# Kernel tuning notes

Measured on AMD Instinct MI355X. Metric: run time of the kernel, lower is better.

## Reference

```python
import jax, jax.numpy as jnp
import numpy as np

EPS = 1e-6
DIM_HEAD = 32
INP = 128
OUP = 128
IH = IW = 32


def _conv3x3(x, w):
    # NCHW conv, 3x3, stride 1, pad 1, no bias
    return jax.lax.conv_general_dilated(
        x, w, window_strides=(1, 1), padding=((1, 1), (1, 1)),
        dimension_numbers=("NCHW", "OIHW", "NCHW"))


def _groupnorm1(x, gamma, beta):
    # GroupNorm with 1 group: normalize over (C,H,W) per sample
    m = jnp.mean(x, axis=(1, 2, 3), keepdims=True)
    v = jnp.var(x, axis=(1, 2, 3), keepdims=True)
    xn = (x - m) * jax.lax.rsqrt(v + EPS)
    return xn * gamma[None, :, None, None] + beta[None, :, None, None]


def _proj(x, w, gamma, beta):
    return jax.nn.gelu(_groupnorm1(_conv3x3(x, w), gamma, beta), approximate=False)


def _relative_index(ih, iw):
    coords = np.stack(np.meshgrid(np.arange(ih), np.arange(iw), indexing="ij"))
    coords = coords.reshape(2, -1)  # (2, N)
    rel = coords[:, :, None] - coords[:, None, :]  # (2, N, N)
    rel[0] += ih - 1
    rel[1] += iw - 1
    rel[0] *= 2 * iw - 1
    return rel.sum(0).reshape(-1).astype(np.int32)  # (N*N,)


def setup_inputs() -> dict:
    key = jax.random.key(0)
    ks = jax.random.split(key, 12)
    B = 16
    x = jax.random.normal(ks[0], (B, INP, IH, IW), jnp.float32)
    w_scale = 0.05
    wq = jax.random.normal(ks[1], (INP, INP, 3, 3), jnp.float32) * w_scale
    wk = jax.random.normal(ks[2], (INP, INP, 3, 3), jnp.float32) * w_scale
    wv = jax.random.normal(ks[3], (INP, INP, 3, 3), jnp.float32) * w_scale
    gq = jnp.ones((INP,), jnp.float32); bq = jnp.zeros((INP,), jnp.float32)
    gk = jnp.ones((INP,), jnp.float32); bk = jnp.zeros((INP,), jnp.float32)
    gv = jnp.ones((INP,), jnp.float32); bv = jnp.zeros((INP,), jnp.float32)
    heads = INP // DIM_HEAD
    table = jax.random.normal(ks[4], ((2 * IH - 1) * (2 * IW - 1), heads), jnp.float32) * 0.02
    rel_index = jnp.asarray(_relative_index(IH, IW))
    out_w = jax.random.normal(ks[5], (OUP, INP, 1, 1), jnp.float32) * w_scale
    out_b = jnp.zeros((OUP,), jnp.float32)
    return {"x": x, "wq": wq, "gq": gq, "bq": bq, "wk": wk, "gk": gk, "bk": bk,
            "wv": wv, "gv": gv, "bv": bv, "table": table, "rel_index": rel_index,
            "out_w": out_w, "out_b": out_b}


def reference(x, wq, gq, bq, wk, gk, bk, wv, gv, bv, table, rel_index, out_w, out_b):
    B, C, ih, iw = x.shape
    H = C // DIM_HEAD
    N = ih * iw

    def to_heads(t):
        # b c ih iw -> b (ihiw) c -> b h n d (heads-major channel split)
        return t.reshape(B, C, N).transpose(0, 2, 1).reshape(B, N, H, DIM_HEAD).transpose(0, 2, 1, 3)

    q = to_heads(_proj(x, wq, gq, bq))
    k = to_heads(_proj(x, wk, gk, bk))
    v = to_heads(_proj(x, wv, gv, bv))

    # NOTE: original applies self.scale only when y is not None; y=None here -> no scale
    dots = jnp.einsum("bhnd,bhmd->bhnm", q, k)  # (B,H,N,N)

    bias = table[rel_index]                 # (N*N, H)
    bias = bias.reshape(N, N, H).transpose(2, 0, 1)[None]  # (1,H,N,N)
    attn = jax.nn.softmax(dots + bias, axis=-1)

    out = jnp.einsum("bhnm,bhmd->bhnd", attn, v)
    out = out.transpose(0, 2, 1, 3).reshape(B, N, C).transpose(0, 2, 1).reshape(B, C, ih, iw)
    # to_out: 1x1 conv + bias (Dropout2d is identity in eval)
    out = jax.lax.conv_general_dilated(
        out, out_w, window_strides=(1, 1), padding=((0, 0), (0, 0)),
        dimension_numbers=("NCHW", "OIHW", "NCHW")) + out_b[None, :, None, None]
    return out
```

## Files before the change

### kernel.cpp

```cpp
#include <hip/hip_runtime.h>

typedef unsigned short u16;
typedef unsigned int   u32;

#define NB   16
#define NC   128
#define NPIX 1024
#define NH   4
#define DH   32

typedef __attribute__((ext_vector_type(8))) short short8;
typedef __attribute__((ext_vector_type(4))) float f32x4;
typedef __attribute__((ext_vector_type(8))) _Float16 half8;

#define XROWS 1152

__device__ __forceinline__ float bf2f(u16 u) {
    return __uint_as_float(((u32)u) << 16);
}
__device__ __forceinline__ u16 f2bf(float f) {
    u32 u = __float_as_uint(f);
    u32 r = (u + 0x7fffu + ((u >> 16) & 1u)) >> 16;
    return (u16)r;
}
__device__ __forceinline__ u16 f2h(float f) {
    _Float16 h = (_Float16)f;
    u16 r; __builtin_memcpy(&r, &h, 2); return r;
}
__device__ __forceinline__ float h2f(u16 u) {
    _Float16 h; __builtin_memcpy(&h, &u, 2); return (float)h;
}
__device__ __forceinline__ int pk_h2(float a, float b) {
    auto h = __builtin_amdgcn_cvt_pkrtz(a, b);
    int r; __builtin_memcpy(&r, &h, 4); return r;
}
__device__ __forceinline__ float loadf(const void* p, int i, int isf) {
    return isf ? ((const float*)p)[i] : bf2f(((const u16*)p)[i]);
}
__device__ __forceinline__ float4 load4(const void* p, int i4, int isf) {
    if (isf) return ((const float4*)p)[i4];
    ushort4 u = ((const ushort4*)p)[i4];
    return make_float4(bf2f(u.x), bf2f(u.y), bf2f(u.z), bf2f(u.w));
}
__device__ __forceinline__ int detect_isf(const void* x) {
    const u16* p = (const u16*)x;
    u16 v = p[threadIdx.x & 63];
    int e = (v >> 7) & 0xFF;
    unsigned long long m = __ballot(e >= 134);
    return m != 0ull ? 1 : 0;
}

__global__ __launch_bounds__(256) void prep_all(
        const void* __restrict__ x,
        const void* __restrict__ w0, const void* __restrict__ w1,
        const void* __restrict__ w2, const void* __restrict__ ow,
        const int* __restrict__ rel, const void* __restrict__ table,
        u16* __restrict__ Wt, u16* __restrict__ Wf, u16* __restrict__ xTp,
        u16* __restrict__ biasT, float* __restrict__ stats) {
    __shared__ __align__(16) u32 smem_u[4160];
    int isf = detect_isf(x);
    int bid = blockIdx.x;
    int t = threadIdx.x;

    if (bid < 1792) {
        if (bid == 0 && t < 96) stats[t] = 0.f;
        int i = bid * 256 + t;
        if (i < 442368) {
            int j   = i / 147456;
            int rr  = i % 147456;
            int tap = rr >> 14;
            int co  = (rr >> 7) & 127;
            int ci  = rr & 127;
            const void* w = (j == 0) ? w0 : ((j == 1) ? w1 : w2);
            float v = loadf(w, (co * 128 + ci) * 9 + tap, isf);
            int coh = (co >> 6) & 1, wm = (co >> 5) & 1;
            int mt  = (co >> 4) & 1, l16 = co & 15;
            int ks  = (ci >> 5) & 3, q  = (ci >> 3) & 3, e = ci & 7;
            int dst = (j * 9 + tap) * 16384
                    + (coh * 2 + wm) * 4096 + ks * 1024 + mt * 512
                    + (q * 16 + l16) * 8 + e;
            Wt[dst] = f2bf(v);
        } else {
            int i2 = i - 442368;
            if (i2 < 16384) {
                int co = i2 >> 7, k = i2 & 127;
                int zc = (co >> 6) & 1, wm = (co >> 5) & 1;
                int mt = (co >> 4) & 1, l16 = co & 15;
                int ks = (k >> 5) & 3, q = (k >> 3) & 3, e = k & 7;
                int dst = (zc * 2 + wm) * 4096 + ks * 1024 + mt * 512
                        + (q * 16 + l16) * 8 + e;
                Wf[dst] = f2h(loadf(ow, i2, isf));
            }
        }
    } else if (bid < 2304) {
        float* tile = (float*)smem_u;
        int b2 = bid - 1792;
        int pixg = b2 & 7, cig = (b2 >> 3) & 3, b = b2 >> 5;

        if (pixg == 0 || pixg == 7) {
            int row = (pixg == 0 ? 0 : 1088) + (t >> 2);
            int seg = t & 3;
            size_t dst = ((size_t)(b * XROWS + row)) * 128 + cig * 32 + seg * 8;
            *(uint4*)&xTp[dst] = make_uint4(0, 0, 0, 0);
        }

        int ci = t >> 3, px0 = (t & 7) * 16;
        int base = b * (NC * NPIX) + (cig * 32 + ci) * NPIX + pixg * 128 + px0;
#pragma unroll
        for (int u = 0; u < 4; ++u) {
            float4 v = load4(x, (base >> 2) + u, isf);
            float* d = &tile[ci * 129 + px0 + u * 4];
            d[0] = v.x; d[1] = v.y; d[2] = v.z; d[3] = v.w;
        }
        __syncthreads();
#pragma unroll
        for (int u = 0; u < 2; ++u) {
            int c = t + u * 256;
            int pix = c >> 2, seg = c & 3;
            u16 tmp[8];
#pragma unroll
            for (int e = 0; e < 8; ++e)
                tmp[e] = f2bf(tile[(seg * 8 + e) * 129 + pix]);
            size_t dst = ((size_t)(b * XROWS + 64 + pixg * 128 + pix)) * 128
                       + cig * 32 + seg * 8;
            *(ushort4*)&xTp[dst] =
                make_ushort4(tmp[0], tmp[1], tmp[2], tmp[3]);
            *(ushort4*)&xTp[dst + 4] =
                make_ushort4(tmp[4], tmp[5], tmp[6], tmp[7]);
        }
    } else {
        int* rl = (int*)smem_u;
        int b2 = bid - 2304;
        int nt = b2 & 15, mt = b2 >> 4;

#pragma unroll
        for (int c = 0; c < 16; ++c) {
            int i = t + c * 256;
            int r = i >> 6, cc = i & 63;
            rl[r * 65 + cc] = rel[(size_t)(nt * 64 + r) * 1024 + mt * 64 + cc];
        }
        __syncthreads();

#pragma unroll
        for (int h = 0; h < NH; ++h) {
#pragma unroll
            for (int c = 0; c < 16; ++c) {
                int wdx = t + c * 256;
                int r     = wdx & 3;
                int lane  = (wdx >> 2) & 63;
                int fragl = wdx >> 8;
                int n16l  = fragl >> 2;
                int m16l  = fragl & 3;
                int n_loc = n16l * 16 + (lane & 15);
                int m_loc = m16l * 16 + ((lane >> 4) << 2) + r;
                int ri = rl[n_loc * 65 + m_loc];
                float v = loadf(table, ri * NH + h, isf);
                biasT[((size_t)h << 20)
                      + ((size_t)((nt * 4 + n16l) * 64 + (mt * 4 + m16l)) << 8)
                      + lane * 4 + r] = f2bf(v);
            }
        }
    }
}

__global__ __launch_bounds__(256) void conv6_kernel(
        const u16* __restrict__ xTp, const u16* __restrict__ Wt,
        u16* __restrict__ conv_out, float* __restrict__ stats) {
    __shared__ __align__(16) u16 Xh[194 * 128];

    int t = threadIdx.x;
    int bx = blockIdx.x, b = blockIdx.y, j = blockIdx.z;
    int pt = bx >> 1, coh = bx & 1;
    int p0 = pt * 128;
    int w = t >> 6, lane = t & 63;
    int q = lane >> 4, l16 = lane & 15;
    int cobase = coh * 64 + (w & 1) * 32;
    int pixbase = (w >> 1) * 64;

    const u16* xb  = xTp + ((size_t)b * XROWS + 64) * 128;
    const u16* wrb = Wt + (size_t)(j * 9) * 16384
                   + (coh * 2 + (w & 1)) * 4096 + lane * 8;

    short8 awA[2][4], awB[2][4];
#pragma unroll
    for (int ks = 0; ks < 4; ++ks) {
        awA[0][ks] = *(const short8*)(wrb + ks * 1024);
        awA[1][ks] = *(const short8*)(wrb + ks * 1024 + 512);
    }

#pragma unroll
    for (int k = 0; k < 13; ++k) {
        int c = t + k * 256;
        if (c < 194 * 16) {
            int row = c >> 4, seg = c & 15;
            int pg = p0 - 33 + row;
            uint4 v = *(const uint4*)(xb + (size_t)pg * 128 + seg * 8);
            *(uint4*)&Xh[row * 128 + ((seg + row) & 15) * 8] = v;
        }
    }
    __syncthreads();

    f32x4 acc[2][4];
#pragma unroll
    for (int mt = 0; mt < 2; ++mt)
#pragma unroll
        for (int nt = 0; nt < 4; ++nt) acc[mt][nt] = (f32x4)0.f;

#pragma unroll
    for (int tap = 0; tap < 9; ++tap) {
        const int dy = tap / 3, dx = tap % 3;
        bool inv_e = (dx == 0) && (l16 == 0);
        bool inv_o = (dx == 2) && (l16 == 15);
        int rbase = pixbase + dy * 32 + dx + l16;

        if (tap < 8) {
            const u16* nw = wrb + (size_t)(tap + 1) * 16384;
            if ((tap & 1) == 0) {
#pragma unroll
                for (int ks = 0; ks < 4; ++ks) {
                    awB[0][ks] = *(const short8*)(nw + ks * 1024);
                    awB[1][ks] = *(const short8*)(nw + ks * 1024 + 512);
                }
            } else {
#pragma unroll
                for (int ks = 0; ks < 4; ++ks) {
                    awA[0][ks] = *(const short8*)(nw + ks * 1024);
                    awA[1][ks] = *(const short8*)(nw + ks * 1024 + 512);
                }
            }
        }

#pragma unroll
        for (int ks = 0; ks < 4; ++ks) {
            int sl = ks * 4 + q;
            short8 bf[4];
#pragma unroll
            for (int nt = 0; nt < 4; ++nt) {
                int row = rbase + nt * 16;
                short8 v = *(const short8*)&Xh[row * 128
                                               + ((sl + row) & 15) * 8];
                bf[nt] = ((nt & 1) ? inv_o : inv_e) ? (short8)0 : v;
            }
#pragma unroll
            for (int mt = 0; mt < 2; ++mt) {
                short8 a = ((tap & 1) == 0) ? awA[mt][ks] : awB[mt][ks];
#pragma unroll
                for (int nt = 0; nt < 4; ++nt)
                    acc[mt][nt] = __builtin_amdgcn_mfma_f32_16x16x32_bf16(
                        a, bf[nt], acc[mt][nt], 0, 0, 0);
            }
        }
    }

    float s = 0.f, s2 = 0.f;
    size_t obase = ((size_t)(j * NB + b) * NC) * NPIX;
#pragma unroll
    for (int mt = 0; mt < 2; ++mt) {
#pragma unroll
        for (int nt = 0; nt < 4; ++nt) {
            f32x4 v = acc[mt][nt];
            int co  = cobase + mt * 16 + q * 4;
            int pix = p0 + pixbase + nt * 16 + l16;
#pragma unroll
            for (int r = 0; r < 4; ++r) {
                float val = v[r];
                conv_out[obase + (size_t)(co + r) * NPIX + pix] = f2h(val);
                s += val;
                s2 = fmaf(val, val, s2);
            }
        }
    }
#pragma unroll
    for (int off = 32; off; off >>= 1) {
        s  += __shfl_down(s,  (unsigned)off, 64);
        s2 += __shfl_down(s2, (unsigned)off, 64);
    }
    if (lane == 0) {
        atomicAdd(&stats[(j * NB + b) * 2 + 0], s);
        atomicAdd(&stats[(j * NB + b) * 2 + 1], s2);
    }
}

__global__ __launch_bounds__(256) void norm_kernel(
        const void* __restrict__ xdet,
        const u16* __restrict__ conv_out, const float* __restrict__ stats,
        const void* __restrict__ g0, const void* __restrict__ b0,
        const void* __restrict__ g1, const void* __restrict__ b1,
        const void* __restrict__ g2, const void* __restrict__ b2,
        u16* __restrict__ qh, u16* __restrict__ kh, u16* __restrict__ vh) {
    __shared__ float tile[32 * 257];
    int isf = detect_isf(xdet);
    int t = threadIdx.x;
    int n0 = blockIdx.x * 256;
    int h = blockIdx.y;
    int z = blockIdx.z;
    int j = z >> 4;
    int b = z & 15;
    const void* gam = (j == 0) ? g0 : ((j == 1) ? g1 : g2);
    const void* bet = (j == 0) ? b0 : ((j == 1) ? b1 : b2);

    float sum = stats[z * 2], ss = stats[z * 2 + 1];
    const float inv = 1.0f / 131072.0f;
    float mean = sum * inv;
    float var  = fmaxf(ss * inv - mean * mean, 0.f);
    float rstd = rsqrtf(var + 1e-6f);

    const u16* src = conv_out + ((size_t)z * NC + h * DH) * NPIX + n0;

    if (j == 2) {
        u16* dst = vh + (((size_t)(b * NH + h)) * DH) * NPIX + n0;
#pragma unroll
        for (int cl = 0; cl < 32; ++cl) {
            float v = h2f(src[cl * NPIX + t]);
            v = (v - mean) * rstd * loadf(gam, h * DH + cl, isf)
              + loadf(bet, h * DH + cl, isf);
            v = 0.5f * v * (1.0f + erff(v * 0.70710678118654752f));
            dst[(size_t)cl * NPIX + t] = f2h(v);
        }
        return;
    }

#pragma unroll
    for (int cl = 0; cl < 32; ++cl)
        tile[cl * 257 + t] = h2f(src[cl * NPIX + t]);
    __syncthreads();

    u16* dst = ((j == 0) ? qh : kh)
             + (((size_t)(b * NH + h)) * NPIX + n0) * DH;
#pragma unroll
    for (int k = 0; k < 32; ++k) {
        int o = t + k * 256;
        int d = o & 31, nl = o >> 5;
        float v = tile[d * 257 + nl];
        v = (v - mean) * rstd * loadf(gam, h * DH + d, isf)
          + loadf(bet, h * DH + d, isf);
        v = 0.5f * v * (1.0f + erff(v * 0.70710678118654752f));
        dst[o] = f2h(v);
    }
}

__global__ __launch_bounds__(256) void attn2_kernel(
        const u16* __restrict__ qh, const u16* __restrict__ kh,
        const u16* __restrict__ vh, const u16* __restrict__ biasT,
        u16* __restrict__ attfh) {
    __shared__ __align__(16) u16 Kl[2][128 * 40];
    __shared__ __align__(16) u16 Vl[2][32 * 136];

    int t = threadIdx.x;
    int f = blockIdx.x;
    int r_ = f >> 3;
    int g = (f & 7) * 4 + (r_ >> 4);
    int b = r_ & 15;
    int h = g & 3, qt = g >> 2;
    int w = t >> 6, lane = t & 63, q = lane >> 4, l16 = lane & 15;
    int nrow0 = qt * 128 + w * 32;

    const u16* qb = qh + (((size_t)(b * NH + h)) * NPIX) * DH;
    const u16* kb = kh + (((size_t)(b * NH + h)) * NPIX) * DH;
    const u16* vb = vh + (((size_t)(b * NH + h)) * DH) * NPIX;
    const u16* bf0 = biasT + ((size_t)h << 20)
                   + ((size_t)(qt * 8 + w * 2 + 0) << 14) + lane * 4;
    const u16* bf1 = biasT + ((size_t)h << 20)
                   + ((size_t)(qt * 8 + w * 2 + 1) << 14) + lane * 4;

    int krow = t >> 2, kseg = t & 3;
    int vrow = t >> 4, vseg = t & 15;

    {
        uint4 k0 = *(const uint4*)(kb + t * 8);
        uint4 k1 = *(const uint4*)(kb + (t + 256) * 8);
        uint4 v0 = *(const uint4*)(vb + vrow * NPIX + vseg * 8);
        uint4 v1 = *(const uint4*)(vb + (vrow + 16) * NPIX + vseg * 8);
        *(uint4*)&Kl[0][krow * 40 + kseg * 8] = k0;
        *(uint4*)&Kl[0][(krow + 64) * 40 + kseg * 8] = k1;
        *(uint4*)&Vl[0][vrow * 136 + vseg * 8] = v0;
        *(uint4*)&Vl[0][(vrow + 16) * 136 + vseg * 8] = v1;
    }

    half8 qf[2];
#pragma unroll
    for (int nt = 0; nt < 2; ++nt)
        qf[nt] = *(const half8*)(qb + (size_t)(nrow0 + nt * 16 + l16) * DH
                                 + q * 8);

    f32x4 O[2][2];
#pragma unroll
    for (int dt = 0; dt < 2; ++dt)
#pragma unroll
        for (int nt = 0; nt < 2; ++nt) O[dt][nt] = (f32x4)0.f;
    float mrow[2] = {-1e30f, -1e30f}, lrow[2] = {0.f, 0.f};

    __syncthreads();

    for (int kc = 0; kc < 8; ++kc) {
        int cur = kc & 1;
        const u16* Kc = &Kl[cur][0];
        const u16* Vc = &Vl[cur][0];

        uint4 pk0, pk1, pv0, pv1;
        bool pf = (kc < 7);
        if (pf) {
            int m0n = (kc + 1) * 128;
            pk0 = *(const uint4*)(kb + m0n * 32 + t * 8);
            pk1 = *(const uint4*)(kb + m0n * 32 + (t + 256) * 8);
            pv0 = *(const uint4*)(vb + vrow * NPIX + m0n + vseg * 8);
            pv1 = *(const uint4*)(vb + (vrow + 16) * NPIX + m0n + vseg * 8);
        }

        f32x4 St[8][2];
#pragma unroll
        for (int mt = 0; mt < 8; ++mt) {
            half8 kf = *(const half8*)&Kc[(mt * 16 + l16) * 40 + q * 8];
            int m16 = kc * 8 + mt;
            ushort4 bv0 = *(const ushort4*)(bf0 + (m16 << 8));
            ushort4 bv1 = *(const ushort4*)(bf1 + (m16 << 8));
            f32x4 c0, c1;
            c0[0] = bf2f(bv0.x); c0[1] = bf2f(bv0.y);
            c0[2] = bf2f(bv0.z); c0[3] = bf2f(bv0.w);
            c1[0] = bf2f(bv1.x); c1[1] = bf2f(bv1.y);
            c1[2] = bf2f(bv1.z); c1[3] = bf2f(bv1.w);
            St[mt][0] = __builtin_amdgcn_mfma_f32_16x16x32_f16(
                kf, qf[0], c0, 0, 0, 0);
            St[mt][1] = __builtin_amdgcn_mfma_f32_16x16x32_f16(
                kf, qf[1], c1, 0, 0, 0);
        }
        float mx[2] = {-1e30f, -1e30f};
#pragma unroll
        for (int mt = 0; mt < 8; ++mt)
#pragma unroll
            for (int nt = 0; nt < 2; ++nt)
#pragma unroll
                for (int r = 0; r < 4; ++r)
                    mx[nt] = fmaxf(mx[nt], St[mt][nt][r]);
        float alpha[2];
#pragma unroll
        for (int nt = 0; nt < 2; ++nt) {
            mx[nt] = fmaxf(mx[nt], __shfl_xor(mx[nt], 16, 64));
            mx[nt] = fmaxf(mx[nt], __shfl_xor(mx[nt], 32, 64));
            float mn = fmaxf(mrow[nt], mx[nt]);
            alpha[nt] = __expf(mrow[nt] - mn);
            mrow[nt] = mn;
        }
        float sm[2] = {0.f, 0.f};
#pragma unroll
        for (int mt = 0; mt < 8; ++mt)
#pragma unroll
            for (int nt = 0; nt < 2; ++nt)
#pragma unroll
                for (int r = 0; r < 4; ++r) {
                    float p = __expf(St[mt][nt][r] - mrow[nt]);
                    St[mt][nt][r] = p;
                    sm[nt] += p;
                }
#pragma unroll
        for (int nt = 0; nt < 2; ++nt) {
            sm[nt] += __shfl_xor(sm[nt], 16, 64);
            sm[nt] += __shfl_xor(sm[nt], 32, 64);
            lrow[nt] = lrow[nt] * alpha[nt] + sm[nt];
        }
        if (!__all(alpha[0] == 1.0f && alpha[1] == 1.0f)) {
#pragma unroll
            for (int dt = 0; dt < 2; ++dt)
#pragma unroll
                for (int nt = 0; nt < 2; ++nt)
#pragma unroll
                    for (int r = 0; r < 4; ++r)
                        O[dt][nt][r] *= alpha[nt];
        }
#pragma unroll
        for (int ms = 0; ms < 4; ++ms) {
            half8 vf[2];
#pragma unroll
            for (int dt = 0; dt < 2; ++dt) {
                const u16* vrow_p = &Vc[(dt * 16 + l16) * 136 + ms * 32];
                uint2 lo = *(const uint2*)(vrow_p + q * 4);
                uint2 hi = *(const uint2*)(vrow_p + 16 + q * 4);
                uint4 cmb = make_uint4(lo.x, lo.y, hi.x, hi.y);
                __builtin_memcpy(&vf[dt], &cmb, 16);
            }
#pragma unroll
            for (int nt = 0; nt < 2; ++nt) {
                int pw[4];
                pw[0] = pk_h2(St[2 * ms][nt][0],     St[2 * ms][nt][1]);
                pw[1] = pk_h2(St[2 * ms][nt][2],     St[2 * ms][nt][3]);
                pw[2] = pk_h2(St[2 * ms + 1][nt][0], St[2 * ms + 1][nt][1]);
                pw[3] = pk_h2(St[2 * ms + 1][nt][2], St[2 * ms + 1][nt][3]);
                half8 pf2; __builtin_memcpy(&pf2, pw, 16);
#pragma unroll
                for (int dt = 0; dt < 2; ++dt)
                    O[dt][nt] = __builtin_amdgcn_mfma_f32_16x16x32_f16(
                        vf[dt], pf2, O[dt][nt], 0, 0, 0);
            }
        }
        if (pf) {
            *(uint4*)&Kl[cur ^ 1][krow * 40 + kseg * 8] = pk0;
            *(uint4*)&Kl[cur ^ 1][(krow + 64) * 40 + kseg * 8] = pk1;
            *(uint4*)&Vl[cur ^ 1][vrow * 136 + vseg * 8] = pv0;
            *(uint4*)&Vl[cur ^ 1][(vrow + 16) * 136 + vseg * 8] = pv1;
        }
        __syncthreads();
    }

#pragma unroll
    for (int nt = 0; nt < 2; ++nt) {
        float rl = 1.0f / lrow[nt];
        int n = nrow0 + nt * 16 + l16;
        u16* dst = attfh + ((size_t)b * NPIX + n) * NC + h * DH;
#pragma unroll
        for (int dt = 0; dt < 2; ++dt) {
            f32x4 o = O[dt][nt];
            uint2 pv = make_uint2((u32)pk_h2(o[0] * rl, o[1] * rl),
                                  (u32)pk_h2(o[2] * rl, o[3] * rl));
            *(uint2*)(dst + dt * 16 + q * 4) = pv;
        }
    }
}

__global__ __launch_bounds__(256) void out3_kernel(
        const void* __restrict__ xdet,
        const u16* __restrict__ attfh, const u16* __restrict__ Wf,
        const void* __restrict__ ob, void* __restrict__ out) {
    int isf = detect_isf(xdet);
    int t = threadIdx.x;
    int n0 = blockIdx.x * 64, b = blockIdx.y, zc = blockIdx.z;
    int w = t >> 6, lane = t & 63, q = lane >> 4, l16 = lane & 15;
    int cobase = zc * 64 + (w & 1) * 32, nbase = (w >> 1) * 32;

    f32x4 acc[2][2];
#pragma unroll
    for (int mt = 0; mt < 2; ++mt)
#pragma unroll
        for (int nt = 0; nt < 2; ++nt) acc[mt][nt] = (f32x4)0.f;

    const u16* ab = attfh + ((size_t)b * NPIX + n0 + nbase) * NC;
    const u16* wfb = Wf + (zc * 2 + (w & 1)) * 4096 + lane * 8;
#pragma unroll
    for (int ks = 0; ks < 4; ++ks) {
        int k0 = ks * 32 + q * 8;
        half8 a[2], bfr[2];
#pragma unroll
        for (int mt = 0; mt < 2; ++mt)
            a[mt] = *(const half8*)(wfb + ks * 1024 + mt * 512);
#pragma unroll
        for (int nt = 0; nt < 2; ++nt)
            bfr[nt] = *(const half8*)(ab + (size_t)(nt * 16 + l16) * NC + k0);
#pragma unroll
        for (int mt = 0; mt < 2; ++mt)
#pragma unroll
            for (int nt = 0; nt < 2; ++nt)
                acc[mt][nt] = __builtin_amdgcn_mfma_f32_16x16x32_f16(
                    a[mt], bfr[nt], acc[mt][nt], 0, 0, 0);
    }

#pragma unroll
    for (int mt = 0; mt < 2; ++mt) {
#pragma unroll
        for (int nt = 0; nt < 2; ++nt) {
            f32x4 v = acc[mt][nt];
            int n = n0 + nbase + nt * 16 + l16;
#pragma unroll
            for (int r = 0; r < 4; ++r) {
                int co = cobase + mt * 16 + q * 4 + r;
                float val = v[r] + loadf(ob, co, isf);
                size_t oidx = ((size_t)b * NC + co) * NPIX + n;
                if (isf) ((float*)out)[oidx] = val;
                else     ((u16*)out)[oidx]   = f2bf(val);
            }
        }
    }
}

extern "C" void kernel_launch(void* const* d_in, const int* in_sizes, int n_in,
                              void* d_out, int out_size, void* d_ws,
                              size_t ws_size, hipStream_t stream) {
    (void)in_sizes; (void)n_in; (void)out_size; (void)ws_size;
    const void* x     = d_in[0];
    const void* wq    = d_in[1];
    const void* gq    = d_in[2];
    const void* bq    = d_in[3];
    const void* wk    = d_in[4];
    const void* gk    = d_in[5];
    const void* bk    = d_in[6];
    const void* wv    = d_in[7];
    const void* gv    = d_in[8];
    const void* bv    = d_in[9];
    const void* table = d_in[10];
    const int*  rel   = (const int*)d_in[11];
    const void* ow    = d_in[12];
    const void* ob    = d_in[13];

    char* ws = (char*)d_ws;
    float* stats = (float*)(ws);
    char*  regQ  = ws + 512;
    u16*   xTp   = (u16*)regQ;
    u16*   Wt    = (u16*)(regQ + 5242880);
    u16*   qhp   = (u16*)regQ;
    u16*   khp   = (u16*)(regQ + 4194304);
    u16*   vhp   = (u16*)(regQ + 8388608);
    u16*   biasT = (u16*)(regQ + 12582912);
    u16*   Wf    = (u16*)(regQ + 20971520);
    char*  regA  = regQ + 25165824;
    u16*   conv  = (u16*)regA;
    u16*   attfh = (u16*)(regA + 16777216);

    prep_all<<<2560, 256, 0, stream>>>(x, wq, wk, wv, ow, rel, table,
                                       Wt, Wf, xTp, biasT, stats);
    conv6_kernel<<<dim3(16, 16, 3), 256, 0, stream>>>(xTp, Wt, conv, stats);
    norm_kernel<<<dim3(4, 4, 48), 256, 0, stream>>>(x, conv, stats,
                                                    gq, bq, gk, bk, gv, bv,
                                                    qhp, khp, vhp);
    attn2_kernel<<<512, 256, 0, stream>>>(qhp, khp, vhp, biasT, attfh);
    out3_kernel<<<dim3(16, 16, 2), 256, 0, stream>>>(x, attfh, Wf, ob, d_out);
}
```

Baseline: 192.4 us.

## Store conv output in MFMA fragment layout and vectorize norm kernel access

The conv kernel now writes each MFMA accumulator fragment as one packed 8-byte store into a fragment-tiled intermediate layout instead of scattered 2-byte stores. The norm kernel reads that layout directly with 8-byte loads, drops the shared-memory transpose tile and barrier, and writes Q/K with packed 8-byte stores. V is still written with scalar stores. This changes the intermediate layout contract between the two kernels and how the norm grid maps onto blocks, so correctness depends on the blockIdx.x range matching the new 16x16 fragment tiling.

```diff
diff --git a/kernel.cpp b/kernel.cpp
--- a/kernel.cpp
+++ b/kernel.cpp
@@ -253,21 +253,28 @@
     }
 
     float s = 0.f, s2 = 0.f;
-    size_t obase = ((size_t)(j * NB + b) * NC) * NPIX;
+    int z = j * NB + b;
+    int co16b  = coh * 4 + (w & 1) * 2;
+    int pix16b = pt * 8 + (w >> 1) * 4;
 #pragma unroll
     for (int mt = 0; mt < 2; ++mt) {
 #pragma unroll
         for (int nt = 0; nt < 4; ++nt) {
             f32x4 v = acc[mt][nt];
-            int co  = cobase + mt * 16 + q * 4;
-            int pix = p0 + pixbase + nt * 16 + l16;
+            u16 ev[4];
 #pragma unroll
             for (int r = 0; r < 4; ++r) {
                 float val = v[r];
-                conv_out[obase + (size_t)(co + r) * NPIX + pix] = f2h(val);
+                ev[r] = f2h(val);
                 s += val;
                 s2 = fmaf(val, val, s2);
             }
+            uint2 pw;
+            __builtin_memcpy(&pw, ev, 8);
+            size_t addr = (size_t)z * 131072
+                        + (size_t)(co16b + mt) * 16384
+                        + (size_t)(pix16b + nt) * 256 + lane * 4;
+            *(uint2*)&conv_out[addr] = pw;
         }
     }
 #pragma unroll
@@ -283,15 +290,14 @@
 
 __global__ __launch_bounds__(256) void norm_kernel(
         const void* __restrict__ xdet,
-        const u16* __restrict__ conv_out, const float* __restrict__ stats,
+        const u16* __restrict__ convF, const float* __restrict__ stats,
         const void* __restrict__ g0, const void* __restrict__ b0,
         const void* __restrict__ g1, const void* __restrict__ b1,
         const void* __restrict__ g2, const void* __restrict__ b2,
         u16* __restrict__ qh, u16* __restrict__ kh, u16* __restrict__ vh) {
-    __shared__ float tile[32 * 257];
     int isf = detect_isf(xdet);
     int t = threadIdx.x;
-    int n0 = blockIdx.x * 256;
+    int x = blockIdx.x;
     int h = blockIdx.y;
     int z = blockIdx.z;
     int j = z >> 4;
@@ -305,37 +311,47 @@
     float var  = fmaxf(ss * inv - mean * mean, 0.f);
     float rstd = rsqrtf(var + 1e-6f);
 
-    const u16* src = conv_out + ((size_t)z * NC + h * DH) * NPIX + n0;
-
-    if (j == 2) {
-        u16* dst = vh + (((size_t)(b * NH + h)) * DH) * NPIX + n0;
-#pragma unroll
-        for (int cl = 0; cl < 32; ++cl) {
-            float v = h2f(src[cl * NPIX + t]);
-            v = (v - mean) * rstd * loadf(gam, h * DH + cl, isf)
-              + loadf(bet, h * DH + cl, isf);
-            v = 0.5f * v * (1.0f + erff(v * 0.70710678118654752f));
-            dst[(size_t)cl * NPIX + t] = f2h(v);
-        }
-        return;
-    }
-
-#pragma unroll
-    for (int cl = 0; cl < 32; ++cl)
-        tile[cl * 257 + t] = h2f(src[cl * NPIX + t]);
-    __syncthreads();
-
-    u16* dst = ((j == 0) ? qh : kh)
-             + (((size_t)(b * NH + h)) * NPIX + n0) * DH;
-#pragma unroll
-    for (int k = 0; k < 32; ++k) {
-        int o = t + k * 256;
-        int d = o & 31, nl = o >> 5;
-        float v = tile[d * 257 + nl];
-        v = (v - mean) * rstd * loadf(gam, h * DH + d, isf)
-          + loadf(bet, h * DH + d, isf);
-        v = 0.5f * v * (1.0f + erff(v * 0.70710678118654752f));
-        dst[o] = f2h(v);
+    int lane = t & 63, fi = t >> 6;
+    int q2 = lane >> 4, l16 = lane & 15;
+
+    const size_t zbase = (size_t)z * 131072;
+    u16* qkdst = ((j == 0) ? qh : kh) + ((size_t)(b * NH + h)) * NPIX * DH;
+    u16* vdst  = vh + ((size_t)(b * NH + h)) * DH * NPIX;
+
+#pragma unroll
+    for (int p = 0; p < 8; ++p) {
+        int fgi   = p * 4 + fi;
+        int co16l = fgi >> 4;
+        int pix16l = fgi & 15;
+        int co16  = h * 2 + co16l;
+        int pix16 = x * 16 + pix16l;
+        const u16* src = convF + zbase + (size_t)co16 * 16384
+                       + (size_t)pix16 * 256 + lane * 4;
+        uint2 wv = *(const uint2*)src;
+        u16 ev[4];
+        __builtin_memcpy(ev, &wv, 8);
+
+        int cl0 = co16l * 16 + q2 * 4;
+        int pix = pix16 * 16 + l16;
+
+        float o[4];
+#pragma unroll
+        for (int r = 0; r < 4; ++r) {
+            float v = h2f(ev[r]);
+            v = (v - mean) * rstd * loadf(gam, h * DH + cl0 + r, isf)
+              + loadf(bet, h * DH + cl0 + r, isf);
+            o[r] = 0.5f * v * (1.0f + erff(v * 0.70710678118654752f));
+        }
+
+        if (j == 2) {
+#pragma unroll
+            for (int r = 0; r < 4; ++r)
+                vdst[(size_t)(cl0 + r) * NPIX + pix] = f2h(o[r]);
+        } else {
+            uint2 pw = make_uint2((u32)pk_h2(o[0], o[1]),
+                                  (u32)pk_h2(o[2], o[3]));
+            *(uint2*)(qkdst + (size_t)pix * DH + cl0) = pw;
+        }
     }
 }
 
```

Result: no change. 189.0 us (-1.8%).
